# Kernel tuning notes

Measured on AMD Instinct MI355X. Metric: run time of the kernel, lower is better.

The kernel has to match this reference:

```python
import jax, jax.numpy as jnp
import numpy as np

B, S, HID = 4, 2048, 2048
NH, NKV, HD = 16, 4, 128  # head_dim = HID // NH
Q_SIZE, KV_SIZE = NH * HD, NKV * HD


def setup_inputs() -> dict:
    key = jax.random.key(0)
    ks = jax.random.split(key, 8)
    pos = jnp.arange(S, dtype=jnp.float32)[:, None]
    inv_freq = 1.0 / (10000.0 ** (jnp.arange(0, HD, 2, dtype=jnp.float32) / HD))  # [HD/2]
    ang = pos * inv_freq[None, :]  # [S, HD/2]
    return {
        "hidden_states": jax.random.normal(ks[0], (B, S, HID), jnp.float32),
        "rotary_pos_emb_cos": jnp.cos(ang),
        "rotary_pos_emb_sin": jnp.sin(ang),
        "w_qkv": jax.random.normal(ks[1], (HID, Q_SIZE + 2 * KV_SIZE), jnp.float32) * (HID ** -0.5),
        "b_qkv": jax.random.normal(ks[2], (Q_SIZE + 2 * KV_SIZE,), jnp.float32) * 0.02,
        "w_o": jax.random.normal(ks[3], (HID, HID), jnp.float32) * (HID ** -0.5),
        "b_o": jax.random.normal(ks[4], (HID,), jnp.float32) * 0.02,
    }


def _apply_rope(x, cos, sin):
    # x: [B, S, H, D]; cos/sin: [S, D/2]; rotate-half (non-interleaved) convention
    d2 = x.shape[-1] // 2
    x1, x2 = x[..., :d2], x[..., d2:]
    c = cos[None, :, None, :]
    s = sin[None, :, None, :]
    return jnp.concatenate([x1 * c - x2 * s, x2 * c + x1 * s], axis=-1)


def reference(hidden_states, rotary_pos_emb_cos, rotary_pos_emb_sin, w_qkv, b_qkv, w_o, b_o):
    b, s, _ = hidden_states.shape
    qkv = hidden_states @ w_qkv + b_qkv  # [B, S, Q_SIZE + 2*KV_SIZE]
    q, k, v = jnp.split(qkv, [Q_SIZE, Q_SIZE + KV_SIZE], axis=-1)
    q = q.reshape(b, s, NH, HD)
    k = k.reshape(b, s, NKV, HD)
    v = v.reshape(b, s, NKV, HD)
    q = _apply_rope(q, rotary_pos_emb_cos, rotary_pos_emb_sin)
    k = _apply_rope(k, rotary_pos_emb_cos, rotary_pos_emb_sin)
    # grouped-query attention: repeat kv heads to match query heads
    g = NH // NKV
    k = jnp.repeat(k, g, axis=2)  # [B, S, NH, HD]
    v = jnp.repeat(v, g, axis=2)
    scale = HD ** -0.5
    scores = jnp.einsum("bshd,bthd->bhst", q, k) * scale  # [B, NH, S, S]
    probs = jax.nn.softmax(scores, axis=-1)
    out = jnp.einsum("bhst,bthd->bshd", probs, v)  # [B, S, NH, HD]
    out = out.reshape(b, s, NH * HD)
    return out @ w_o + b_o
```

## Files before the change

### kernel.cpp

```cpp
#include <hip/hip_runtime.h>
#include <math.h>

#define B_N   4
#define S_N   2048
#define HID_N 2048
#define NH_N  16
#define NKV_N 4
#define HD_N  128
#define QSZ   2048
#define KVSZ  512
#define QKVN  3072
#define M_N   8192

typedef __bf16 bf16;
typedef __bf16 bf16x8 __attribute__((ext_vector_type(8)));
typedef float  f32x4  __attribute__((ext_vector_type(4)));

#define GLL16(gp, lp)                                                          \
  __builtin_amdgcn_global_load_lds(                                            \
      (const __attribute__((address_space(1))) void*)(gp),                     \
      (__attribute__((address_space(3))) void*)(lp), 16, 0, 0)

#define CFENCE asm volatile("" ::: "memory")
#define BARRIER do { CFENCE; __builtin_amdgcn_s_barrier(); CFENCE; } while (0)

__device__ __forceinline__ f32x4 mfma16(bf16x8 a, bf16x8 b, f32x4 c) {
  return __builtin_amdgcn_mfma_f32_16x16x32_bf16(a, b, c, 0, 0, 0);
}

__global__ __launch_bounds__(256) void conv_bf16_kernel(
    const float* __restrict__ X, bf16* __restrict__ Y)
{
  size_t i = ((size_t)blockIdx.x * 256 + threadIdx.x) * 8;
  float4 a = *(const float4*)&X[i];
  float4 b = *(const float4*)&X[i + 4];
  union { bf16 h[8]; uint4 u; } pk;
  pk.h[0] = (bf16)a.x; pk.h[1] = (bf16)a.y; pk.h[2] = (bf16)a.z; pk.h[3] = (bf16)a.w;
  pk.h[4] = (bf16)b.x; pk.h[5] = (bf16)b.y; pk.h[6] = (bf16)b.z; pk.h[7] = (bf16)b.w;
  *(uint4*)&Y[i] = pk.u;
}

__global__ __launch_bounds__(256) void convT_kernel(
    const float* __restrict__ W, bf16* __restrict__ Wt, int K, int N)
{
  __shared__ __attribute__((aligned(16))) bf16 tile[64 * 68];
  const int n0 = blockIdx.x * 64, k0 = blockIdx.y * 64;
#pragma unroll
  for (int it = 0; it < 4; ++it) {
    int idx = it * 256 + threadIdx.x;
    int r = idx >> 4, c4 = (idx & 15) << 2;
    float4 v = *(const float4*)&W[(size_t)(k0 + r) * N + n0 + c4];
    union { bf16 h[4]; unsigned long long u; } pk;
    pk.h[0] = (bf16)v.x; pk.h[1] = (bf16)v.y; pk.h[2] = (bf16)v.z; pk.h[3] = (bf16)v.w;
    *(unsigned long long*)&tile[r * 68 + c4] = pk.u;
  }
  __syncthreads();
#pragma unroll
  for (int it = 0; it < 4; ++it) {
    int idx = it * 256 + threadIdx.x;
    int rn = idx >> 4, ck4 = (idx & 15) << 2;
    union { bf16 h[4]; unsigned long long u; } pk;
#pragma unroll
    for (int i = 0; i < 4; ++i) pk.h[i] = tile[(ck4 + i) * 68 + rn];
    *(unsigned long long*)&Wt[(size_t)(n0 + rn) * K + k0 + ck4] = pk.u;
  }
}

template <bool OUT_BF16>
__global__ __launch_bounds__(512, 2) void gemm256_kernel(
    const bf16* __restrict__ A, const bf16* __restrict__ Bt,
    const float* __restrict__ bias, void* __restrict__ Cout,
    int M, int N, int K, int nbx)
{
  __shared__ __attribute__((aligned(16))) bf16 Asl[2][2][256 * 32];
  __shared__ __attribute__((aligned(16))) bf16 Bsl[2][2][256 * 32];

  const int tid  = threadIdx.x;
  const int lane = tid & 63, wv = tid >> 6;
  const int quad = lane >> 4, ln = lane & 15;
  const int wm = wv >> 2, wn = wv & 3;

  const int cpx = (int)gridDim.x >> 3;
  const int gid = ((int)blockIdx.x & 7) * cpx + ((int)blockIdx.x >> 3);
  const int row0 = (gid / nbx) * 256, col0 = (gid % nbx) * 256;

  const int slot0 = (wv * 2 + 0) * 64 + lane;
  const int slot1 = (wv * 2 + 1) * 64 + lane;
  const bf16* gA0 = A  + (size_t)(row0 + (slot0 >> 2)) * K + (slot0 & 3) * 8;
  const bf16* gA1 = A  + (size_t)(row0 + (slot1 >> 2)) * K + (slot1 & 3) * 8;
  const bf16* gB0 = Bt + (size_t)(col0 + (slot0 >> 2)) * K + (slot0 & 3) * 8;
  const bf16* gB1 = Bt + (size_t)(col0 + (slot1 >> 2)) * K + (slot1 & 3) * 8;
  const int lu0 = (wv * 2 + 0) * 512, lu1 = (wv * 2 + 1) * 512;

#define STG_A(buf, kh, t) do {                                               \
    GLL16(gA0 + (size_t)(t) * 64 + (kh) * 32, &Asl[buf][kh][lu0]);           \
    GLL16(gA1 + (size_t)(t) * 64 + (kh) * 32, &Asl[buf][kh][lu1]);           \
  } while (0)
#define STG_B(buf, kh, t) do {                                               \
    GLL16(gB0 + (size_t)(t) * 64 + (kh) * 32, &Bsl[buf][kh][lu0]);           \
    GLL16(gB1 + (size_t)(t) * 64 + (kh) * 32, &Bsl[buf][kh][lu1]);           \
  } while (0)

  f32x4 acc[8][4];
  const f32x4 zero = {0.f, 0.f, 0.f, 0.f};
#pragma unroll
  for (int mf = 0; mf < 8; ++mf)
#pragma unroll
    for (int nf = 0; nf < 4; ++nf) acc[mf][nf] = zero;

  bf16x8 a[4], bfr[2][4];
  const int NT = K >> 6;

  STG_B(0, 0, 0); STG_B(0, 1, 0); STG_A(0, 0, 0); STG_A(0, 1, 0);
  STG_B(1, 0, 1); STG_B(1, 1, 1); STG_A(1, 0, 1);
  CFENCE; asm volatile("s_waitcnt vmcnt(6)" ::: "memory");
  BARRIER;

#define PH(mh, kh, READ_B, STAGE_STMT, WAIT_STMT) do {                       \
    const bf16* Ab = &Asl[cur][kh][(wm * 128 + (mh) * 64 + ln) * 32 + quad * 8]; \
    _Pragma("unroll")                                                        \
    for (int mf = 0; mf < 4; ++mf)                                           \
      a[mf] = *(const bf16x8*)(Ab + mf * 16 * 32);                           \
    if (READ_B) {                                                            \
      const bf16* Bb = &Bsl[cur][kh][(wn * 64 + ln) * 32 + quad * 8];        \
      _Pragma("unroll")                                                      \
      for (int nf = 0; nf < 4; ++nf)                                         \
        bfr[kh][nf] = *(const bf16x8*)(Bb + nf * 16 * 32);                   \
    }                                                                        \
    STAGE_STMT;                                                              \
    BARRIER;                                                                 \
    __builtin_amdgcn_s_setprio(1);                                           \
    _Pragma("unroll")                                                        \
    for (int mf = 0; mf < 4; ++mf)                                           \
      _Pragma("unroll")                                                      \
      for (int nf = 0; nf < 4; ++nf)                                         \
        acc[(mh) * 4 + mf][nf] = mfma16(a[mf], bfr[kh][nf],                  \
                                        acc[(mh) * 4 + mf][nf]);             \
    __builtin_amdgcn_s_setprio(0);                                           \
    WAIT_STMT;                                                               \
    BARRIER;                                                                 \
  } while (0)

  int cur = 0;
  for (int t = 0; t < NT; ++t, cur ^= 1) {
    PH(0, 0, 1, { if (t + 1 < NT) STG_A(cur ^ 1, 1, t + 1); }, {});
    PH(0, 1, 1, { if (t + 2 < NT) STG_B(cur, 0, t + 2); },     {});
    PH(1, 0, 0, { if (t + 2 < NT) STG_B(cur, 1, t + 2); },     {});
    PH(1, 1, 0, { if (t + 2 < NT) STG_A(cur, 0, t + 2); },
       { if (t == NT - 2) { asm volatile("s_waitcnt vmcnt(0)" ::: "memory"); } \
         else if (t < NT - 2) { asm volatile("s_waitcnt vmcnt(6)" ::: "memory"); } });
  }
#undef PH
#undef STG_A
#undef STG_B

#pragma unroll
  for (int nf = 0; nf < 4; ++nf) {
    const int c = col0 + wn * 64 + nf * 16 + ln;
    const float bv = bias[c];
#pragma unroll
    for (int mf = 0; mf < 8; ++mf) {
#pragma unroll
      for (int r = 0; r < 4; ++r) {
        const int rr = row0 + wm * 128 + mf * 16 + quad * 4 + r;
        const float v = acc[mf][nf][r] + bv;
        if (OUT_BF16) ((bf16*)Cout)[(size_t)rr * N + c] = (bf16)v;
        else          ((float*)Cout)[(size_t)rr * N + c] = v;
      }
    }
  }
}

__global__ __launch_bounds__(256) void rope_repack_kernel(
    const bf16* __restrict__ qkvB, const float* __restrict__ cosb,
    const float* __restrict__ sinb, bf16* __restrict__ Qb, bf16* __restrict__ Kb)
{
  int idx = blockIdx.x * 256 + threadIdx.x;
  int j  = idx & 63;
  int m  = (idx >> 6) & (M_N - 1);
  int hh = idx >> 19;
  int b = m >> 11, s = m & (S_N - 1);
  float c  = cosb[s * 64 + j];
  float sn = sinb[s * 64 + j];
  if (hh < NH_N) {
    const bf16* src = qkvB + (size_t)m * QKVN + hh * HD_N;
    float x1 = (float)src[j], x2 = (float)src[j + 64];
    bf16* dst = Qb + ((size_t)(b * NH_N + hh) * S_N + s) * HD_N;
    const float qs = 0.08838834764831845f * 1.4426950408889634f;
    dst[j]      = (bf16)((x1 * c - x2 * sn) * qs);
    dst[j + 64] = (bf16)((x2 * c + x1 * sn) * qs);
  } else {
    int kh = hh - NH_N;
    const bf16* src = qkvB + (size_t)m * QKVN + QSZ + kh * HD_N;
    float x1 = (float)src[j], x2 = (float)src[j + 64];
    bf16* dst = Kb + ((size_t)(b * NKV_N + kh) * S_N + s) * HD_N;
    dst[j]      = (bf16)(x1 * c - x2 * sn);
    dst[j + 64] = (bf16)(x2 * c + x1 * sn);
  }
}

__global__ __launch_bounds__(256) void transposeV_kernel(
    const bf16* __restrict__ qkvB, bf16* __restrict__ Vt)
{
  __shared__ __attribute__((aligned(16))) bf16 tile[64 * 136];
  const int s0 = blockIdx.x * 64;
  const int bkh = blockIdx.y;
  const int b = bkh >> 2, kh = bkh & 3;
#pragma unroll
  for (int it = 0; it < 4; ++it) {
    int ci = it * 256 + threadIdx.x;
    int r = ci >> 4, c = ci & 15;
    uint4 v = *(const uint4*)&qkvB[(size_t)(b * S_N + s0 + r) * QKVN +
                                   QSZ + KVSZ + kh * HD_N + c * 8];
    *(uint4*)&tile[r * 136 + c * 8] = v;
  }
  __syncthreads();
#pragma unroll
  for (int it = 0; it < 4; ++it) {
    int ci = it * 256 + threadIdx.x;
    int d = ci >> 3, c = ci & 7;
    union { bf16 h[8]; uint4 u; } pk;
#pragma unroll
    for (int i = 0; i < 8; ++i) pk.h[i] = tile[(c * 8 + i) * 136 + d];
    *(uint4*)&Vt[((size_t)bkh * HD_N + d) * S_N + s0 + c * 8] = pk.u;
  }
}

__global__ __launch_bounds__(256, 3) void attn_mfma_kernel(
    const bf16* __restrict__ Qb, const bf16* __restrict__ Kb,
    const bf16* __restrict__ Vt, bf16* __restrict__ Ob)
{
  __shared__ __attribute__((aligned(16))) bf16 Ks[2][32 * 128];
  __shared__ __attribute__((aligned(16))) bf16 Vs[2][128 * 32];
  __shared__ __attribute__((aligned(16))) bf16 Ps[128 * 40];

  const int tid  = threadIdx.x;
  const int lane = tid & 63, wv = tid >> 6;
  const int quad = lane >> 4, ln = lane & 15;

  const int gid = blockIdx.x;
  const int xcd = gid & 7, sl = gid >> 3;
  const int grp = xcd * 2 + (sl >> 6);
  const int within = sl & 63;
  const int b = grp >> 2, kh = grp & 3;
  const int h = kh * 4 + (within >> 4);
  const int q0 = (within & 15) * 128;

  const bf16* Qg = Qb + ((size_t)(b * NH_N + h) * S_N + q0) * HD_N;
  const bf16* Kg = Kb + (size_t)(b * NKV_N + kh) * S_N * HD_N;
  const bf16* Vg = Vt + (size_t)(b * NKV_N + kh) * HD_N * S_N;

  bf16x8 aq[2][4];
#pragma unroll
  for (int g = 0; g < 2; ++g) {
    const bf16* qrow = Qg + (size_t)((wv * 2 + g) * 16 + ln) * HD_N;
#pragma unroll
    for (int dc = 0; dc < 4; ++dc)
      aq[g][dc] = *(const bf16x8*)&qrow[(dc * 4 + quad) * 8];
  }

  const bf16* kga[2];
  const bf16* vga[2];
#pragma unroll
  for (int t = 0; t < 2; ++t) {
    int slot = (t * 4 + wv) * 64 + lane;
    int row = slot >> 4, cc = slot & 15;
    int csrc = (cc & 8) | ((cc & 7) ^ (row & 7));
    kga[t] = Kg + (size_t)row * 128 + csrc * 8;
    int dv = slot >> 2, ccv = slot & 3;
    int csv = ccv ^ ((dv >> 1) & 3);
    vga[t] = Vg + (size_t)dv * S_N + csv * 8;
  }

#pragma unroll
  for (int t = 0; t < 2; ++t) GLL16(kga[t], &Ks[0][(t * 4 + wv) * 512]);
#pragma unroll
  for (int t = 0; t < 2; ++t) GLL16(vga[t], &Vs[0][(t * 4 + wv) * 512]);

  bf16x8 bones;
#pragma unroll
  for (int j = 0; j < 8; ++j) bones[j] = (ln == 0) ? (bf16)1.0f : (bf16)0.0f;

  f32x4 accO[2][8];
  const f32x4 zero = {0.f, 0.f, 0.f, 0.f};
#pragma unroll
  for (int g = 0; g < 2; ++g)
#pragma unroll
    for (int dt = 0; dt < 8; ++dt) accO[g][dt] = zero;
  f32x4 accL[2] = {zero, zero};

  __syncthreads();

  int cur = 0;
  for (int kt = 0; kt < S_N; kt += 32, cur ^= 1) {
    const int nkt = kt + 32;
    if (nkt < S_N) {
#pragma unroll
      for (int t = 0; t < 2; ++t)
        GLL16(kga[t] + (size_t)nkt * 128, &Ks[cur ^ 1][(t * 4 + wv) * 512]);
#pragma unroll
      for (int t = 0; t < 2; ++t)
        GLL16(vga[t] + nkt, &Vs[cur ^ 1][(t * 4 + wv) * 512]);
    }
    const bf16* Kc = Ks[cur];
    const bf16* Vc = Vs[cur];

    f32x4 accS[2][2];
#pragma unroll
    for (int g = 0; g < 2; ++g)
#pragma unroll
      for (int nt = 0; nt < 2; ++nt) accS[g][nt] = zero;
#pragma unroll
    for (int nt = 0; nt < 2; ++nt) {
      const int kp = nt * 16 + ln;
#pragma unroll
      for (int dc = 0; dc < 4; ++dc) {
        int c = dc * 4 + quad;
        int cs = (c & 8) | ((c & 7) ^ (kp & 7));
        bf16x8 bk = *(const bf16x8*)&Kc[kp * 128 + cs * 8];
        accS[0][nt] = mfma16(aq[0][dc], bk, accS[0][nt]);
        accS[1][nt] = mfma16(aq[1][dc], bk, accS[1][nt]);
      }
    }

#pragma unroll
    for (int g = 0; g < 2; ++g)
#pragma unroll
      for (int r = 0; r < 4; ++r) {
        const int q = (wv * 2 + g) * 16 + quad * 4 + r;
        bf16* pr = &Ps[q * 40 + ln];
        pr[0]  = (bf16)__builtin_amdgcn_exp2f(accS[g][0][r]);
        pr[16] = (bf16)__builtin_amdgcn_exp2f(accS[g][1][r]);
      }

    bf16x8 ap[2];
#pragma unroll
    for (int g = 0; g < 2; ++g) {
      ap[g] = *(const bf16x8*)&Ps[((wv * 2 + g) * 16 + ln) * 40 + quad * 8];
      accL[g] = mfma16(ap[g], bones, accL[g]);
    }
#pragma unroll
    for (int dt = 0; dt < 8; ++dt) {
      const int d = dt * 16 + ln;
      int cs = quad ^ ((d >> 1) & 3);
      bf16x8 bv = *(const bf16x8*)&Vc[d * 32 + cs * 8];
      accO[0][dt] = mfma16(ap[0], bv, accO[0][dt]);
      accO[1][dt] = mfma16(ap[1], bv, accO[1][dt]);
    }

    __syncthreads();
  }

#pragma unroll
  for (int g = 0; g < 2; ++g)
#pragma unroll
    for (int r = 0; r < 4; ++r) {
      const float l = __shfl(accL[g][r], lane & 48);
      const float inv = 1.f / l;
      const int q = q0 + (wv * 2 + g) * 16 + quad * 4 + r;
      const size_t base = ((size_t)b * S_N + q) * HID_N + h * HD_N;
#pragma unroll
      for (int dt = 0; dt < 8; ++dt)
        Ob[base + dt * 16 + ln] = (bf16)(accO[g][dt][r] * inv);
    }
}

extern "C" void kernel_launch(void* const* d_in, const int* in_sizes, int n_in,
                              void* d_out, int out_size, void* d_ws, size_t ws_size,
                              hipStream_t stream) {
  const float* hidden = (const float*)d_in[0];
  const float* cosb   = (const float*)d_in[1];
  const float* sinb   = (const float*)d_in[2];
  const float* w_qkv  = (const float*)d_in[3];
  const float* b_qkv  = (const float*)d_in[4];
  const float* w_o    = (const float*)d_in[5];
  const float* b_o    = (const float*)d_in[6];
  float* out = (float*)d_out;

  char* w = (char*)d_ws;
  bf16* qkvB  = (bf16*)(w);
  bf16* Qb    = (bf16*)(w + 50331648);
  bf16* Kb    = (bf16*)(w + 83886080);
  bf16* Vt    = (bf16*)(w + 92274688);
  bf16* wqkvT = (bf16*)(w + 100663296);
  bf16* woT   = (bf16*)(w + 113246208);
  bf16* hidB  = (bf16*)(w + 121634816);
  bf16* attnB = hidB;

  conv_bf16_kernel<<<(M_N * HID_N) / (256 * 8), 256, 0, stream>>>(hidden, hidB);
  convT_kernel<<<dim3(QKVN / 64, HID_N / 64), 256, 0, stream>>>(w_qkv, wqkvT, HID_N, QKVN);
  convT_kernel<<<dim3(HID_N / 64, HID_N / 64), 256, 0, stream>>>(w_o, woT, HID_N, HID_N);

  gemm256_kernel<true><<<(M_N / 256) * (QKVN / 256), 512, 0, stream>>>(
      hidB, wqkvT, b_qkv, qkvB, M_N, QKVN, HID_N, QKVN / 256);

  rope_repack_kernel<<<(M_N * (NH_N + NKV_N) * 64) / 256, 256, 0, stream>>>(
      qkvB, cosb, sinb, Qb, Kb);
  transposeV_kernel<<<dim3(S_N / 64, B_N * NKV_N), 256, 0, stream>>>(qkvB, Vt);

  attn_mfma_kernel<<<1024, 256, 0, stream>>>(Qb, Kb, Vt, attnB);

  gemm256_kernel<false><<<(M_N / 256) * (HID_N / 256), 512, 0, stream>>>(
      attnB, woT, b_o, out, M_N, HID_N, HID_N, HID_N / 256);
}
```

Baseline: 554.2 us.

## Use XOR-swizzled 64-wide LDS tiles and restage GEMM prefetch schedule

The GEMM's shared-memory tiles change from two 32-wide K halves to a single 64-wide row per buffer, with an XOR swizzle on 16-byte chunks applied on both the global-to-LDS load and the fragment reads. This is meant to cut LDS bank conflicts and use fewer, larger staged loads. The phase order becomes mh-major within each kh, which keeps one B fragment set live instead of two. Most prefetches for step t+2 now issue in the last phase, so the vmcnt accounting and the overlap between loads and MFMA change.

```diff
diff --git a/kernel.cpp b/kernel.cpp
--- a/kernel.cpp
+++ b/kernel.cpp
@@ -72,8 +72,8 @@
     const float* __restrict__ bias, void* __restrict__ Cout,
     int M, int N, int K, int nbx)
 {
-  __shared__ __attribute__((aligned(16))) bf16 Asl[2][2][256 * 32];
-  __shared__ __attribute__((aligned(16))) bf16 Bsl[2][2][256 * 32];
+  __shared__ __attribute__((aligned(16))) bf16 Asl[2][256 * 64];
+  __shared__ __attribute__((aligned(16))) bf16 Bsl[2][256 * 64];
 
   const int tid  = threadIdx.x;
   const int lane = tid & 63, wv = tid >> 6;
@@ -84,22 +84,17 @@
   const int gid = ((int)blockIdx.x & 7) * cpx + ((int)blockIdx.x >> 3);
   const int row0 = (gid / nbx) * 256, col0 = (gid % nbx) * 256;
 
-  const int slot0 = (wv * 2 + 0) * 64 + lane;
-  const int slot1 = (wv * 2 + 1) * 64 + lane;
-  const bf16* gA0 = A  + (size_t)(row0 + (slot0 >> 2)) * K + (slot0 & 3) * 8;
-  const bf16* gA1 = A  + (size_t)(row0 + (slot1 >> 2)) * K + (slot1 & 3) * 8;
-  const bf16* gB0 = Bt + (size_t)(col0 + (slot0 >> 2)) * K + (slot0 & 3) * 8;
-  const bf16* gB1 = Bt + (size_t)(col0 + (slot1 >> 2)) * K + (slot1 & 3) * 8;
-  const int lu0 = (wv * 2 + 0) * 512, lu1 = (wv * 2 + 1) * 512;
-
-#define STG_A(buf, kh, t) do {                                               \
-    GLL16(gA0 + (size_t)(t) * 64 + (kh) * 32, &Asl[buf][kh][lu0]);           \
-    GLL16(gA1 + (size_t)(t) * 64 + (kh) * 32, &Asl[buf][kh][lu1]);           \
-  } while (0)
-#define STG_B(buf, kh, t) do {                                               \
-    GLL16(gB0 + (size_t)(t) * 64 + (kh) * 32, &Bsl[buf][kh][lu0]);           \
-    GLL16(gB1 + (size_t)(t) * 64 + (kh) * 32, &Bsl[buf][kh][lu1]);           \
-  } while (0)
+  const bf16* gAb = A  + (size_t)(row0 + wv * 8 + (lane >> 3)) * K
+                       + (((lane & 7) ^ (lane >> 3)) * 8);
+  const bf16* gBb = Bt + (size_t)(col0 + wv * 8 + (lane >> 3)) * K
+                       + (((lane & 7) ^ (lane >> 3)) * 8);
+
+#define STG_A(buf, U, t)                                                     \
+  GLL16(gAb + (size_t)(U) * 64 * K + (size_t)(t) * 64,                       \
+        &Asl[buf][((U) * 64 + wv * 8) * 64])
+#define STG_B(buf, U, t)                                                     \
+  GLL16(gBb + (size_t)(U) * 64 * K + (size_t)(t) * 64,                       \
+        &Bsl[buf][((U) * 64 + wv * 8) * 64])
 
   f32x4 acc[8][4];
   const f32x4 zero = {0.f, 0.f, 0.f, 0.f};
@@ -108,24 +103,31 @@
 #pragma unroll
     for (int nf = 0; nf < 4; ++nf) acc[mf][nf] = zero;
 
-  bf16x8 a[4], bfr[2][4];
+  bf16x8 a[4], bfr[4];
   const int NT = K >> 6;
 
-  STG_B(0, 0, 0); STG_B(0, 1, 0); STG_A(0, 0, 0); STG_A(0, 1, 0);
-  STG_B(1, 0, 1); STG_B(1, 1, 1); STG_A(1, 0, 1);
-  CFENCE; asm volatile("s_waitcnt vmcnt(6)" ::: "memory");
+  STG_A(0, 0, 0); STG_A(0, 1, 0); STG_A(0, 2, 0); STG_A(0, 3, 0);
+  STG_B(0, 0, 0); STG_B(0, 1, 0); STG_B(0, 2, 0); STG_B(0, 3, 0);
+  if (NT > 1) {
+    STG_A(1, 0, 1); STG_A(1, 2, 1);
+    STG_B(1, 0, 1); STG_B(1, 1, 1); STG_B(1, 2, 1); STG_B(1, 3, 1);
+    CFENCE; asm volatile("s_waitcnt vmcnt(6)" ::: "memory");
+  } else {
+    CFENCE; asm volatile("s_waitcnt vmcnt(0)" ::: "memory");
+  }
   BARRIER;
 
 #define PH(mh, kh, READ_B, STAGE_STMT, WAIT_STMT) do {                       \
-    const bf16* Ab = &Asl[cur][kh][(wm * 128 + (mh) * 64 + ln) * 32 + quad * 8]; \
+    const int csw = (((kh) * 4 + quad) ^ (ln & 7)) * 8;                      \
+    const bf16* Ab = &Asl[cur][(wm * 128 + (mh) * 64 + ln) * 64 + csw];      \
     _Pragma("unroll")                                                        \
     for (int mf = 0; mf < 4; ++mf)                                           \
-      a[mf] = *(const bf16x8*)(Ab + mf * 16 * 32);                           \
+      a[mf] = *(const bf16x8*)(Ab + mf * 16 * 64);                           \
     if (READ_B) {                                                            \
-      const bf16* Bb = &Bsl[cur][kh][(wn * 64 + ln) * 32 + quad * 8];        \
+      const bf16* Bb = &Bsl[cur][(wn * 64 + ln) * 64 + csw];                 \
       _Pragma("unroll")                                                      \
       for (int nf = 0; nf < 4; ++nf)                                         \
-        bfr[kh][nf] = *(const bf16x8*)(Bb + nf * 16 * 32);                   \
+        bfr[nf] = *(const bf16x8*)(Bb + nf * 16 * 64);                       \
     }                                                                        \
     STAGE_STMT;                                                              \
     BARRIER;                                                                 \
@@ -134,7 +136,7 @@
     for (int mf = 0; mf < 4; ++mf)                                           \
       _Pragma("unroll")                                                      \
       for (int nf = 0; nf < 4; ++nf)                                         \
-        acc[(mh) * 4 + mf][nf] = mfma16(a[mf], bfr[kh][nf],                  \
+        acc[(mh) * 4 + mf][nf] = mfma16(a[mf], bfr[nf],                      \
                                         acc[(mh) * 4 + mf][nf]);             \
     __builtin_amdgcn_s_setprio(0);                                           \
     WAIT_STMT;                                                               \
@@ -143,12 +145,17 @@
 
   int cur = 0;
   for (int t = 0; t < NT; ++t, cur ^= 1) {
-    PH(0, 0, 1, { if (t + 1 < NT) STG_A(cur ^ 1, 1, t + 1); }, {});
-    PH(0, 1, 1, { if (t + 2 < NT) STG_B(cur, 0, t + 2); },     {});
-    PH(1, 0, 0, { if (t + 2 < NT) STG_B(cur, 1, t + 2); },     {});
-    PH(1, 1, 0, { if (t + 2 < NT) STG_A(cur, 0, t + 2); },
-       { if (t == NT - 2) { asm volatile("s_waitcnt vmcnt(0)" ::: "memory"); } \
-         else if (t < NT - 2) { asm volatile("s_waitcnt vmcnt(6)" ::: "memory"); } });
+    PH(0, 0, 1,
+       { if (t + 1 < NT) { STG_A(cur ^ 1, 1, t + 1); STG_A(cur ^ 1, 3, t + 1); } },
+       {});
+    PH(1, 0, 0, {}, {});
+    PH(0, 1, 1, {}, {});
+    PH(1, 1, 0,
+       { if (t + 2 < NT) { STG_A(cur, 0, t + 2); STG_A(cur, 2, t + 2);
+                           STG_B(cur, 0, t + 2); STG_B(cur, 1, t + 2);
+                           STG_B(cur, 2, t + 2); STG_B(cur, 3, t + 2); } },
+       { if (t + 2 < NT) { asm volatile("s_waitcnt vmcnt(6)" ::: "memory"); } \
+         else if (t + 2 == NT) { asm volatile("s_waitcnt vmcnt(0)" ::: "memory"); } });
   }
 #undef PH
 #undef STG_A
```

After: 546.1 us. Within noise of the previous version (-1.5%).
